# Kernel optimization log

Hardware: AMD Instinct MI355X
Metric: run time of the kernel (lower is better)

Reference implementation:

```python
import jax, jax.numpy as jnp
import numpy as np

N, E, NMASK, NC = 50000, 600000, 10000, 16
DIMS = [128, 96, 64]
EPS = 1e-5


def _sage(x, src, dst, ew, deg_pos, Wp, bp, Ws, Wn, b):
    # DGL SAGEConv 'pool': m_e = relu(fc_pool(h_src)) * w_e ; neigh = max_e->v m_e
    p = jax.nn.relu(x @ Wp.T + bp)              # [N, din]
    m = p[src] * ew[:, None]                    # [E, din]
    neigh = jax.ops.segment_max(m, dst, num_segments=N)
    neigh = jnp.where(deg_pos, neigh, 0.0)      # zero in-degree -> 0 (DGL convention)
    return jax.nn.relu(x @ Ws.T + neigh @ Wn.T + b)


def setup_inputs() -> dict:
    key = jax.random.key(0)
    ks = iter(jax.random.split(key, 64))
    inp = {}
    inp["x"] = jax.random.normal(next(ks), (N, DIMS[0]), jnp.float32)
    inp["src"] = jax.random.randint(next(ks), (E,), 0, N)
    inp["dst"] = jax.random.randint(next(ks), (E,), 0, N)
    inp["ew"] = jax.random.uniform(next(ks), (E,), jnp.float32)
    inp["mask_nodes"] = jax.random.permutation(next(ks), N)[:NMASK]
    inp["mask_token"] = jax.random.normal(next(ks), (1, DIMS[0]), jnp.float32) * 0.02

    def lin(k, o, i):
        return jax.random.normal(k, (o, i), jnp.float32) * (1.0 / np.sqrt(i))

    enc_pairs = list(zip(DIMS[:-1], DIMS[1:]))              # (128,96),(96,64)
    dec_pairs = [(o, i) for (i, o) in reversed(enc_pairs)]  # (64,96),(96,128)
    for name, pairs in (("enc", enc_pairs), ("dec", dec_pairs)):
        for l, (di, do) in enumerate(pairs):
            inp[f"{name}{l}_Wp"] = lin(next(ks), di, di)
            inp[f"{name}{l}_bp"] = jnp.zeros((di,), jnp.float32)
            inp[f"{name}{l}_Ws"] = lin(next(ks), do, di)
            inp[f"{name}{l}_Wn"] = lin(next(ks), do, di)
            inp[f"{name}{l}_b"] = jnp.zeros((do,), jnp.float32)
    H = DIMS[-1]
    inp["W_e2d"] = lin(next(ks), H, H)
    inp["Wnp"] = lin(next(ks), NC, H)
    inp["bnp"] = jnp.zeros((NC,), jnp.float32)
    inp["ln_g"] = jnp.ones((NC,), jnp.float32)
    inp["ln_b"] = jnp.zeros((NC,), jnp.float32)
    return inp


def reference(x, src, dst, ew, mask_nodes, mask_token,
              enc0_Wp, enc0_bp, enc0_Ws, enc0_Wn, enc0_b,
              enc1_Wp, enc1_bp, enc1_Ws, enc1_Wn, enc1_b,
              dec0_Wp, dec0_bp, dec0_Ws, dec0_Wn, dec0_b,
              dec1_Wp, dec1_bp, dec1_Ws, dec1_Wn, dec1_b,
              W_e2d, Wnp, bnp, ln_g, ln_b):
    deg = jax.ops.segment_sum(jnp.ones((E,), jnp.float32), dst, num_segments=N)
    deg_pos = (deg > 0)[:, None]
    # mask: out_x[mask]=0 then += enc_mask_token  ==  set to token row
    h = x.at[mask_nodes].set(mask_token[0])
    h = _sage(h, src, dst, ew, deg_pos, enc0_Wp, enc0_bp, enc0_Ws, enc0_Wn, enc0_b)
    h = _sage(h, src, dst, ew, deg_pos, enc1_Wp, enc1_bp, enc1_Ws, enc1_Wn, enc1_b)
    # dropout(p=0) is identity
    z = h @ Wnp.T + bnp                              # node_pred linear
    mu = jnp.mean(z, -1, keepdims=True)
    var = jnp.var(z, -1, keepdims=True)
    n_scores = (z - mu) * jax.lax.rsqrt(var + EPS) * ln_g + ln_b
    r = h @ W_e2d.T                                  # encoder_to_decoder (no bias)
    r = _sage(r, src, dst, ew, deg_pos, dec0_Wp, dec0_bp, dec0_Ws, dec0_Wn, dec0_b)
    r = _sage(r, src, dst, ew, deg_pos, dec1_Wp, dec1_bp, dec1_Ws, dec1_Wn, dec1_b)
    return (r[mask_nodes], x[mask_nodes], n_scores)
```

## Files before the change

kernel.cpp:

```cpp
#include <hip/hip_runtime.h>

#define EPS_LN 1e-5f

typedef __attribute__((ext_vector_type(4))) float f32x4;
typedef __attribute__((ext_vector_type(4))) int i32x4;

__device__ inline unsigned short f2bf_rne(float x) {
  unsigned int u = __float_as_uint(x);
  unsigned int r = u + 0x7fffu + ((u >> 16) & 1u);
  return (unsigned short)(r >> 16);
}

__device__ inline float4 bf4_to_f4(uint2 u) {
  float4 f;
  f.x = __uint_as_float(u.x << 16);
  f.y = __uint_as_float(u.x & 0xffff0000u);
  f.z = __uint_as_float(u.y << 16);
  f.w = __uint_as_float(u.y & 0xffff0000u);
  return f;
}

__device__ inline uint2 f4_to_bf4(float4 v) {
  uint2 o;
  o.x = (unsigned)f2bf_rne(v.x) | ((unsigned)f2bf_rne(v.y) << 16);
  o.y = (unsigned)f2bf_rne(v.z) | ((unsigned)f2bf_rne(v.w) << 16);
  return o;
}

__global__ __launch_bounds__(256) void copy_bf16_kernel(const float4* __restrict__ in,
                                                        uint2* __restrict__ out, int n4) {
  int i = blockIdx.x * 256 + threadIdx.x;
  if (i < n4) out[i] = f4_to_bf4(in[i]);
}

__global__ __launch_bounds__(256) void mask_scatter_kernel(const int* __restrict__ mn,
                                                           const float* __restrict__ token,
                                                           unsigned short* __restrict__ H,
                                                           int nmask) {
  int gid = blockIdx.x * 256 + threadIdx.x;
  if (gid >= nmask * 32) return;
  int i = gid >> 5;
  int c4 = (gid & 31) << 2;
  int r = mn[i];
  float4 t = *(const float4*)(token + c4);
  *(uint2*)(H + (size_t)r * 128 + c4) = f4_to_bf4(t);
}

__global__ __launch_bounds__(256) void hist_kernel(const int* __restrict__ dst,
                                                   int* __restrict__ deg, int nE) {
  int e = blockIdx.x * 256 + threadIdx.x;
  if (e < nE) atomicAdd(deg + dst[e], 1);
}

#define SCAN_CHUNK 1024

__global__ __launch_bounds__(256) void blocksum_kernel(const int* __restrict__ deg,
                                                       int* __restrict__ bsum, int n) {
  __shared__ int red[256];
  int base = blockIdx.x * SCAN_CHUNK;
  int tid = threadIdx.x;
  int s = 0;
#pragma unroll
  for (int t = 0; t < SCAN_CHUNK / 256; ++t) {
    int g = base + tid + t * 256;
    if (g < n) s += deg[g];
  }
  red[tid] = s;
  __syncthreads();
  for (int ofs = 128; ofs > 0; ofs >>= 1) {
    if (tid < ofs) red[tid] += red[tid + ofs];
    __syncthreads();
  }
  if (tid == 0) bsum[blockIdx.x] = red[0];
}

__global__ __launch_bounds__(64) void bscan_kernel(const int* __restrict__ bsum,
                                                   int* __restrict__ bbase,
                                                   int* __restrict__ off_n, int nb) {
  int tid = threadIdx.x;
  int v = (tid < nb) ? bsum[tid] : 0;
  int incl = v;
#pragma unroll
  for (int ofs = 1; ofs < 64; ofs <<= 1) {
    int u = __shfl_up(incl, ofs, 64);
    if (tid >= ofs) incl += u;
  }
  if (tid < nb) bbase[tid] = incl - v;
  if (tid == nb - 1) off_n[0] = incl;
}

__global__ __launch_bounds__(256) void chunkscan_kernel(const int* __restrict__ deg,
                                                        const int* __restrict__ bbase,
                                                        int* __restrict__ off, int n) {
  __shared__ int part[256];
  int tid = threadIdx.x;
  int base = blockIdx.x * SCAN_CHUNK;
  int g0 = base + tid * 4;
  int loc[4];
  int s = 0;
#pragma unroll
  for (int j = 0; j < 4; ++j) {
    int g = g0 + j;
    int d = (g < n) ? deg[g] : 0;
    loc[j] = s;
    s += d;
  }
  part[tid] = s;
  __syncthreads();
  for (int ofs = 1; ofs < 256; ofs <<= 1) {
    int v = 0;
    if (tid >= ofs) v = part[tid - ofs];
    __syncthreads();
    if (tid >= ofs) part[tid] += v;
    __syncthreads();
  }
  int pre = (tid == 0) ? 0 : part[tid - 1];
  int b = bbase[blockIdx.x] + pre;
#pragma unroll
  for (int j = 0; j < 4; ++j) {
    int g = g0 + j;
    if (g < n) off[g] = b + loc[j];
  }
}

__global__ __launch_bounds__(256) void scatter_kernel(const int* __restrict__ src,
                                                      const int* __restrict__ dst,
                                                      const float* __restrict__ ew,
                                                      const int* __restrict__ off,
                                                      int* __restrict__ cur,
                                                      int2* __restrict__ esw, int nE) {
  int e = blockIdx.x * 256 + threadIdx.x;
  if (e >= nE) return;
  int d = dst[e];
  int pos = off[d] + atomicAdd(cur + d, 1);
  esw[pos] = make_int2(src[e], __float_as_int(ew[e]));
}

__global__ __launch_bounds__(256) void neigh_csr_kernel(
    const unsigned short* __restrict__ P, const int* __restrict__ off,
    const int2* __restrict__ esw,
    unsigned short* __restrict__ neigh, int din, int lanes, int nN) {
  int gid = blockIdx.x * 256 + threadIdx.x;
  int v = gid / lanes;
  int c = (gid - v * lanes) << 3;
  if (v >= nN) return;
  int jlo = off[v], jhi = off[v + 1];
  float m[8];
#pragma unroll
  for (int t = 0; t < 8; ++t) m[t] = 0.f;
  float n1[8], n2[8], n3[8];
#pragma unroll
  for (int t = 0; t < 8; ++t) { n1[t] = 0.f; n2[t] = 0.f; n3[t] = 0.f; }
  int j = jlo;
  for (; j + 4 <= jhi; j += 4) {
    int2 e0 = esw[j], e1 = esw[j + 1], e2 = esw[j + 2], e3 = esw[j + 3];
    uint4 q0 = *(const uint4*)(P + (size_t)e0.x * din + c);
    uint4 q1 = *(const uint4*)(P + (size_t)e1.x * din + c);
    uint4 q2 = *(const uint4*)(P + (size_t)e2.x * din + c);
    uint4 q3 = *(const uint4*)(P + (size_t)e3.x * din + c);
    float w0 = __int_as_float(e0.y), w1 = __int_as_float(e1.y);
    float w2 = __int_as_float(e2.y), w3 = __int_as_float(e3.y);
    float4 a0 = bf4_to_f4(make_uint2(q0.x, q0.y)), b0 = bf4_to_f4(make_uint2(q0.z, q0.w));
    float4 a1 = bf4_to_f4(make_uint2(q1.x, q1.y)), b1 = bf4_to_f4(make_uint2(q1.z, q1.w));
    float4 a2 = bf4_to_f4(make_uint2(q2.x, q2.y)), b2 = bf4_to_f4(make_uint2(q2.z, q2.w));
    float4 a3 = bf4_to_f4(make_uint2(q3.x, q3.y)), b3 = bf4_to_f4(make_uint2(q3.z, q3.w));
    m[0] = fmaxf(m[0], a0.x * w0); m[1] = fmaxf(m[1], a0.y * w0);
    m[2] = fmaxf(m[2], a0.z * w0); m[3] = fmaxf(m[3], a0.w * w0);
    m[4] = fmaxf(m[4], b0.x * w0); m[5] = fmaxf(m[5], b0.y * w0);
    m[6] = fmaxf(m[6], b0.z * w0); m[7] = fmaxf(m[7], b0.w * w0);
    n1[0] = fmaxf(n1[0], a1.x * w1); n1[1] = fmaxf(n1[1], a1.y * w1);
    n1[2] = fmaxf(n1[2], a1.z * w1); n1[3] = fmaxf(n1[3], a1.w * w1);
    n1[4] = fmaxf(n1[4], b1.x * w1); n1[5] = fmaxf(n1[5], b1.y * w1);
    n1[6] = fmaxf(n1[6], b1.z * w1); n1[7] = fmaxf(n1[7], b1.w * w1);
    n2[0] = fmaxf(n2[0], a2.x * w2); n2[1] = fmaxf(n2[1], a2.y * w2);
    n2[2] = fmaxf(n2[2], a2.z * w2); n2[3] = fmaxf(n2[3], a2.w * w2);
    n2[4] = fmaxf(n2[4], b2.x * w2); n2[5] = fmaxf(n2[5], b2.y * w2);
    n2[6] = fmaxf(n2[6], b2.z * w2); n2[7] = fmaxf(n2[7], b2.w * w2);
    n3[0] = fmaxf(n3[0], a3.x * w3); n3[1] = fmaxf(n3[1], a3.y * w3);
    n3[2] = fmaxf(n3[2], a3.z * w3); n3[3] = fmaxf(n3[3], a3.w * w3);
    n3[4] = fmaxf(n3[4], b3.x * w3); n3[5] = fmaxf(n3[5], b3.y * w3);
    n3[6] = fmaxf(n3[6], b3.z * w3); n3[7] = fmaxf(n3[7], b3.w * w3);
  }
  for (; j < jhi; ++j) {
    int2 e = esw[j];
    float w = __int_as_float(e.y);
    uint4 q = *(const uint4*)(P + (size_t)e.x * din + c);
    float4 a = bf4_to_f4(make_uint2(q.x, q.y)), b = bf4_to_f4(make_uint2(q.z, q.w));
    m[0] = fmaxf(m[0], a.x * w); m[1] = fmaxf(m[1], a.y * w);
    m[2] = fmaxf(m[2], a.z * w); m[3] = fmaxf(m[3], a.w * w);
    m[4] = fmaxf(m[4], b.x * w); m[5] = fmaxf(m[5], b.y * w);
    m[6] = fmaxf(m[6], b.z * w); m[7] = fmaxf(m[7], b.w * w);
  }
#pragma unroll
  for (int t = 0; t < 8; ++t) m[t] = fmaxf(fmaxf(m[t], n1[t]), fmaxf(n2[t], n3[t]));
  uint2 o0 = f4_to_bf4(make_float4(m[0], m[1], m[2], m[3]));
  uint2 o1 = f4_to_bf4(make_float4(m[4], m[5], m[6], m[7]));
  *(uint4*)(neigh + (size_t)v * din + c) = make_uint4(o0.x, o0.y, o1.x, o1.y);
}

__global__ __launch_bounds__(256) void matmul_small_kernel(const float* __restrict__ A,
                                                           const float* __restrict__ B,
                                                           float* __restrict__ C,
                                                           int M, int K, int N) {
  int idx = blockIdx.x * 256 + threadIdx.x;
  if (idx >= M * N) return;
  int o = idx / N, i = idx - o * N;
  float s = 0.f;
  for (int k = 0; k < K; ++k) s += A[o * K + k] * B[k * N + i];
  C[idx] = s;
}

__device__ inline void mfma_b16(f32x4& acc, i32x4 a, i32x4 b) {
  asm volatile("v_mfma_f32_16x16x32_bf16 %0, %1, %2, %0"
               : "+v"(acc)
               : "v"(a), "v"(b));
}

__device__ inline void split_bf16(float x, unsigned short& hi, unsigned short& lo) {
  unsigned int bits = __float_as_uint(x);
  hi = (unsigned short)(bits >> 16);
  float hif = __uint_as_float((unsigned int)hi << 16);
  float res = x - hif;
  lo = (unsigned short)(__float_as_uint(res) >> 16);
}

struct SplitWArgs {
  const float* src[12];
  unsigned short* dh[12];
  unsigned short* dl[12];
  int n[12];
};

__global__ __launch_bounds__(256) void split_w_kernel(SplitWArgs a) {
  int m = blockIdx.y;
  int i = (blockIdx.x * 256 + threadIdx.x) * 4;
  if (i >= a.n[m]) return;
  float4 v = *(const float4*)(a.src[m] + i);
  unsigned short h[4], l[4];
  split_bf16(v.x, h[0], l[0]);
  split_bf16(v.y, h[1], l[1]);
  split_bf16(v.z, h[2], l[2]);
  split_bf16(v.w, h[3], l[3]);
  *(uint2*)(a.dh[m] + i) = make_uint2((unsigned)h[0] | ((unsigned)h[1] << 16),
                                      (unsigned)h[2] | ((unsigned)h[3] << 16));
  *(uint2*)(a.dl[m] + i) = make_uint2((unsigned)l[0] | ((unsigned)l[1] << 16),
                                      (unsigned)l[2] | ((unsigned)l[3] << 16));
}

template <int TNT>
__global__ __launch_bounds__(256) void mfma_gemm_kernel(
    const unsigned short* __restrict__ A1, const unsigned short* __restrict__ Wh1,
    const unsigned short* __restrict__ Wl1, int k1,
    const unsigned short* __restrict__ A2, const unsigned short* __restrict__ Wh2,
    const unsigned short* __restrict__ Wl2, int k2,
    const float* __restrict__ bias, int relu,
    unsigned short* __restrict__ C, int nrows) {
  constexpr int BN = TNT * 16;
  constexpr int WS = 136;
  __shared__ __align__(16) unsigned short Wh[BN][WS];
  __shared__ __align__(16) unsigned short Wl[BN][WS];

  const int tid = threadIdx.x;
  const int lane = tid & 63;
  const int wv = tid >> 6;
  const int lr = lane & 15;
  const int lg = lane >> 4;
  const int row0 = blockIdx.x * 64;
  const int gra = row0 + wv * 16 + lr;

  f32x4 acc[TNT];
#pragma unroll
  for (int t = 0; t < TNT; ++t) acc[t] = (f32x4)(0.f);

  for (int pass = 0; pass < 2; ++pass) {
    const unsigned short* A = pass ? A2 : A1;
    if (A == nullptr) continue;
    const unsigned short* Whp = pass ? Wh2 : Wh1;
    const unsigned short* Wlp = pass ? Wl2 : Wl1;
    const int K = pass ? k2 : k1;

    if (pass) __syncthreads();
    {
      int tot8 = BN * K / 8;
      for (int i = tid; i < tot8; i += 256) {
        int e0 = i * 8;
        int col = e0 / K;
        int kk = e0 - col * K;
        *(uint4*)&Wh[col][kk] = *(const uint4*)(Whp + e0);
        *(uint4*)&Wl[col][kk] = *(const uint4*)(Wlp + e0);
      }
    }
    __syncthreads();

    for (int cb = 0; cb < K; cb += 32) {
      i32x4 a_h = (i32x4)(0);
      if (gra < nrows) a_h = *(const i32x4*)(A + (size_t)gra * K + cb + lg * 8);
#pragma unroll
      for (int t = 0; t < TNT; ++t) {
        i32x4 b_h = *(const i32x4*)&Wh[t * 16 + lr][cb + lg * 8];
        i32x4 b_l = *(const i32x4*)&Wl[t * 16 + lr][cb + lg * 8];
        mfma_b16(acc[t], a_h, b_h);
        mfma_b16(acc[t], a_h, b_l);
      }
    }
  }

  asm volatile("s_nop 7\n\ts_nop 7" ::);

#pragma unroll
  for (int t = 0; t < TNT; ++t) {
    int c = t * 16 + lr;
    float bv = bias ? bias[c] : 0.f;
#pragma unroll
    for (int q = 0; q < 4; ++q) {
      int r = row0 + wv * 16 + lg * 4 + q;
      if (r < nrows) {
        float v = acc[t][q] + bv;
        if (relu) v = fmaxf(v, 0.f);
        C[(size_t)r * BN + c] = f2bf_rne(v);
      }
    }
  }
}

__global__ __launch_bounds__(256) void nodepred_ln_kernel(
    const unsigned short* __restrict__ H, const float* __restrict__ Wnp,
    const float* __restrict__ bnp, const float* __restrict__ g,
    const float* __restrict__ lb, float* __restrict__ out, int nrows) {
  __shared__ float hs[16][64];
  int tid = threadIdx.x;
  int row0 = blockIdx.x * 16;
  {
    int r = tid >> 4;
    int c4 = (tid & 15) << 2;
    int gr = row0 + r;
    float4 v = make_float4(0.f, 0.f, 0.f, 0.f);
    if (gr < nrows) v = bf4_to_f4(*(const uint2*)(H + (size_t)gr * 64 + c4));
    *(float4*)&hs[r][c4] = v;
  }
  __syncthreads();
  int r = tid >> 4, j = tid & 15;
  float z = bnp[j];
  const float* wrow = Wnp + j * 64;
#pragma unroll 8
  for (int k = 0; k < 64; ++k) z += hs[r][k] * wrow[k];
  float s = z, s2 = z * z;
#pragma unroll
  for (int m = 1; m < 16; m <<= 1) {
    s += __shfl_xor(s, m, 16);
    s2 += __shfl_xor(s2, m, 16);
  }
  float mu = s * (1.f / 16.f);
  float var = s2 * (1.f / 16.f) - mu * mu;
  float o = (z - mu) * rsqrtf(var + EPS_LN) * g[j] + lb[j];
  int gr = row0 + r;
  if (gr < nrows) out[(size_t)gr * 16 + j] = o;
}

__global__ __launch_bounds__(256) void gather_out_kernel(
    const int* __restrict__ mn, const unsigned short* __restrict__ R,
    const float* __restrict__ X,
    float* __restrict__ o1, float* __restrict__ o2, int nmask) {
  int gid = blockIdx.x * 256 + threadIdx.x;
  if (gid >= nmask * 32) return;
  int i = gid >> 5, c4 = (gid & 31) << 2;
  int r = mn[i];
  float4 rv = bf4_to_f4(*(const uint2*)(R + (size_t)r * 128 + c4));
  *(float4*)(o1 + (size_t)i * 128 + c4) = rv;
  *(float4*)(o2 + (size_t)i * 128 + c4) = *(const float4*)(X + (size_t)r * 128 + c4);
}

static void launch_gemm(const unsigned short* A1, const unsigned short* Wh1,
                        const unsigned short* Wl1, int k1,
                        const unsigned short* A2, const unsigned short* Wh2,
                        const unsigned short* Wl2, int k2,
                        const float* bias, int relu,
                        unsigned short* C, int m, int nrows, hipStream_t s) {
  int blocks = (nrows + 63) / 64;
  switch (m) {
    case 128:
      mfma_gemm_kernel<8><<<blocks, 256, 0, s>>>(A1, Wh1, Wl1, k1, A2, Wh2, Wl2, k2,
                                                 bias, relu, C, nrows);
      break;
    case 96:
      mfma_gemm_kernel<6><<<blocks, 256, 0, s>>>(A1, Wh1, Wl1, k1, A2, Wh2, Wl2, k2,
                                                 bias, relu, C, nrows);
      break;
    case 64:
      mfma_gemm_kernel<4><<<blocks, 256, 0, s>>>(A1, Wh1, Wl1, k1, A2, Wh2, Wl2, k2,
                                                 bias, relu, C, nrows);
      break;
  }
}

extern "C" void kernel_launch(void* const* d_in, const int* in_sizes, int n_in,
                              void* d_out, int out_size, void* d_ws, size_t ws_size,
                              hipStream_t stream) {
  const float* x = (const float*)d_in[0];
  const int* src = (const int*)d_in[1];
  const int* dst = (const int*)d_in[2];
  const float* ew = (const float*)d_in[3];
  const int* mn = (const int*)d_in[4];
  const float* token = (const float*)d_in[5];

  const float* W[20];
  for (int i = 0; i < 20; ++i) W[i] = (const float*)d_in[6 + i];
  const float* W_e2d = (const float*)d_in[26];
  const float* Wnp = (const float*)d_in[27];
  const float* bnp = (const float*)d_in[28];
  const float* ln_g = (const float*)d_in[29];
  const float* ln_b = (const float*)d_in[30];

  const int Nn = in_sizes[0] / 128;
  const int E = in_sizes[1];
  const int nmask = in_sizes[4];
  const int nb = (Nn + SCAN_CHUNK - 1) / SCAN_CHUNK;

  unsigned short* bufA = (unsigned short*)d_ws;
  unsigned short* bufB = bufA + (size_t)Nn * 128;
  unsigned short* pool16 = bufB + (size_t)Nn * 128;
  unsigned short* neigh16 = pool16 + (size_t)Nn * 128;
  int* deg = (int*)(neigh16 + (size_t)Nn * 128);
  int* cur = deg + Nn;
  int2* esw = (int2*)(cur + Nn);
  int* off = (int*)(esw + E);
  int* bsum = off + Nn + 1;
  int* bbase = bsum + 64;
  float* WpP = (float*)(bbase + 64);
  float* WsP = WpP + 64 * 64;
  unsigned short* wplanes =
      (unsigned short*)(((uintptr_t)(WsP + 96 * 64) + 15) & ~(uintptr_t)15);

  matmul_small_kernel<<<(64 * 64 + 255) / 256, 256, 0, stream>>>(W[10], W_e2d, WpP, 64, 64, 64);
  matmul_small_kernel<<<(96 * 64 + 255) / 256, 256, 0, stream>>>(W[12], W_e2d, WsP, 96, 64, 64);

  const int msz[12] = {128 * 128, 96 * 128, 96 * 128, 96 * 96, 64 * 96, 64 * 96,
                       64 * 64,  96 * 64,  96 * 64,  96 * 96, 128 * 96, 128 * 96};
  const float* msrc[12] = {W[0], W[2], W[3], W[5], W[7], W[8],
                           WpP,  WsP,  W[13], W[15], W[17], W[18]};
  int mtot = 0;
  int moff[12];
  for (int i = 0; i < 12; ++i) { moff[i] = mtot; mtot += msz[i]; }
  unsigned short* wh_[12];
  unsigned short* wl_[12];
  SplitWArgs sa;
  for (int i = 0; i < 12; ++i) {
    wh_[i] = wplanes + moff[i];
    wl_[i] = wplanes + mtot + moff[i];
    sa.src[i] = msrc[i];
    sa.dh[i] = wh_[i];
    sa.dl[i] = wl_[i];
    sa.n[i] = msz[i];
  }
  {
    dim3 grid((128 * 128 / 4 + 255) / 256, 12);
    split_w_kernel<<<grid, 256, 0, stream>>>(sa);
  }

  hipMemsetAsync(deg, 0, (size_t)Nn * 2 * sizeof(int), stream);
  hist_kernel<<<(E + 255) / 256, 256, 0, stream>>>(dst, deg, E);
  blocksum_kernel<<<nb, 256, 0, stream>>>(deg, bsum, Nn);
  bscan_kernel<<<1, 64, 0, stream>>>(bsum, bbase, off + Nn, nb);
  chunkscan_kernel<<<nb, 256, 0, stream>>>(deg, bbase, off, Nn);
  scatter_kernel<<<(E + 255) / 256, 256, 0, stream>>>(src, dst, ew, off, cur, esw, E);

  {
    int n4 = Nn * 128 / 4;
    copy_bf16_kernel<<<(n4 + 255) / 256, 256, 0, stream>>>((const float4*)x, (uint2*)bufA, n4);
    mask_scatter_kernel<<<(nmask * 32 + 255) / 256, 256, 0, stream>>>(mn, token, bufA, nmask);
  }

  auto run_sage = [&](int ip, int is, int in_, const float* bp, const float* b,
                      int din, int dout) {
    launch_gemm(bufA, wh_[ip], wl_[ip], din, nullptr, nullptr, nullptr, 0,
                bp, 1, pool16, din, Nn, stream);
    int lanes = din >> 3;
    long long tot = (long long)Nn * lanes;
    int nblocks = (int)((tot + 255) / 256);
    neigh_csr_kernel<<<nblocks, 256, 0, stream>>>(pool16, off, esw, neigh16, din, lanes, Nn);
    launch_gemm(bufA, wh_[is], wl_[is], din, neigh16, wh_[in_], wl_[in_], din,
                b, 1, bufB, dout, Nn, stream);
    unsigned short* t = bufA; bufA = bufB; bufB = t;
  };

  run_sage(0, 1, 2, W[1], W[4], 128, 96);
  run_sage(3, 4, 5, W[6], W[9], 96, 64);

  float* out_r = (float*)d_out;
  float* out_x = out_r + (size_t)nmask * 128;
  float* out_ns = out_x + (size_t)nmask * 128;
  nodepred_ln_kernel<<<(Nn + 15) / 16, 256, 0, stream>>>(bufA, Wnp, bnp, ln_g, ln_b, out_ns, Nn);

  run_sage(6, 7, 8, W[11], W[14], 64, 96);
  run_sage(9, 10, 11, W[16], W[19], 96, 128);

  gather_out_kernel<<<(nmask * 32 + 255) / 256, 256, 0, stream>>>(mn, bufA, x, out_r, out_x, nmask);
}
```

Baseline: 369.1 us.

## Fuse next layer's pool GEMM into combine GEMM and merge prep kernels

Each SAGE layer's combine GEMM now also computes the next layer's pooling projection (relu(h Wp^T + bp)) from the rows it just wrote, so a separate pool GEMM launch is gone and the output tile is re-read while likely still in cache. Several small preprocessing kernels (bf16 copy, histogram, small weight products, block sums, mask scatter, weight splitting) are merged into two multi-role launches to cut launch overhead. The fused epilogue re-reads C from global memory after a threadfence and reloads shared weights, which adds a sync and extra work per block; the chained-kernel fusion also drops flexibility (bias/relu always applied).

```diff
diff --git a/kernel.cpp b/kernel.cpp
--- a/kernel.cpp
+++ b/kernel.cpp
@@ -27,51 +27,129 @@
   return o;
 }
 
-__global__ __launch_bounds__(256) void copy_bf16_kernel(const float4* __restrict__ in,
-                                                        uint2* __restrict__ out, int n4) {
-  int i = blockIdx.x * 256 + threadIdx.x;
-  if (i < n4) out[i] = f4_to_bf4(in[i]);
-}
-
-__global__ __launch_bounds__(256) void mask_scatter_kernel(const int* __restrict__ mn,
-                                                           const float* __restrict__ token,
-                                                           unsigned short* __restrict__ H,
-                                                           int nmask) {
-  int gid = blockIdx.x * 256 + threadIdx.x;
-  if (gid >= nmask * 32) return;
-  int i = gid >> 5;
-  int c4 = (gid & 31) << 2;
-  int r = mn[i];
-  float4 t = *(const float4*)(token + c4);
-  *(uint2*)(H + (size_t)r * 128 + c4) = f4_to_bf4(t);
-}
-
-__global__ __launch_bounds__(256) void hist_kernel(const int* __restrict__ dst,
-                                                   int* __restrict__ deg, int nE) {
-  int e = blockIdx.x * 256 + threadIdx.x;
-  if (e < nE) atomicAdd(deg + dst[e], 1);
+__device__ inline void split_bf16(float x, unsigned short& hi, unsigned short& lo) {
+  unsigned int bits = __float_as_uint(x);
+  hi = (unsigned short)(bits >> 16);
+  float hif = __uint_as_float((unsigned int)hi << 16);
+  float res = x - hif;
+  lo = (unsigned short)(__float_as_uint(res) >> 16);
+}
+
+__device__ inline void mfma_b16(f32x4& acc, i32x4 a, i32x4 b) {
+  asm volatile("v_mfma_f32_16x16x32_bf16 %0, %1, %2, %0"
+               : "+v"(acc)
+               : "v"(a), "v"(b));
+}
+
+struct SplitWArgs {
+  const float* src[12];
+  unsigned short* dh[12];
+  unsigned short* dl[12];
+  int n[12];
+};
+
+struct Prep1Args {
+  const float4* x4; uint2* h_out; int n4; int cb_blocks;
+  const int* dst; int* deg; int nE; int hist_blocks;
+  const float* W10; const float* We2d; float* WpP;
+  const float* W12; float* WsP;
+};
+
+__global__ __launch_bounds__(256) void prep1_kernel(Prep1Args a) {
+  int b = blockIdx.x;
+  int tid = threadIdx.x;
+  if (b < a.cb_blocks) {
+    int i = b * 256 + tid;
+    if (i < a.n4) a.h_out[i] = f4_to_bf4(a.x4[i]);
+    return;
+  }
+  b -= a.cb_blocks;
+  if (b < a.hist_blocks) {
+    int e = b * 256 + tid;
+    if (e < a.nE) atomicAdd(a.deg + a.dst[e], 1);
+    return;
+  }
+  b -= a.hist_blocks;
+  if (b < 16) {
+    int idx = b * 256 + tid;
+    if (idx < 64 * 64) {
+      int o = idx >> 6, i = idx & 63;
+      float s = 0.f;
+      for (int k = 0; k < 64; ++k) s += a.W10[o * 64 + k] * a.We2d[k * 64 + i];
+      a.WpP[idx] = s;
+    }
+    return;
+  }
+  b -= 16;
+  {
+    int idx = b * 256 + tid;
+    if (idx < 96 * 64) {
+      int o = idx >> 6, i = idx & 63;
+      float s = 0.f;
+      for (int k = 0; k < 64; ++k) s += a.W12[o * 64 + k] * a.We2d[k * 64 + i];
+      a.WsP[idx] = s;
+    }
+  }
 }
 
 #define SCAN_CHUNK 1024
 
-__global__ __launch_bounds__(256) void blocksum_kernel(const int* __restrict__ deg,
-                                                       int* __restrict__ bsum, int n) {
+struct Prep2Args {
+  const int* deg; int* bsum; int n; int nb;
+  const int* mn; const float* token; unsigned short* H; int nmask; int ms_blocks;
+  SplitWArgs sw;
+  int boff[13];
+};
+
+__global__ __launch_bounds__(256) void prep2_kernel(Prep2Args a) {
   __shared__ int red[256];
-  int base = blockIdx.x * SCAN_CHUNK;
+  int b = blockIdx.x;
   int tid = threadIdx.x;
-  int s = 0;
-#pragma unroll
-  for (int t = 0; t < SCAN_CHUNK / 256; ++t) {
-    int g = base + tid + t * 256;
-    if (g < n) s += deg[g];
-  }
-  red[tid] = s;
-  __syncthreads();
-  for (int ofs = 128; ofs > 0; ofs >>= 1) {
-    if (tid < ofs) red[tid] += red[tid + ofs];
+  if (b < a.nb) {
+    int base = b * SCAN_CHUNK;
+    int s = 0;
+#pragma unroll
+    for (int t = 0; t < SCAN_CHUNK / 256; ++t) {
+      int g = base + tid + t * 256;
+      if (g < a.n) s += a.deg[g];
+    }
+    red[tid] = s;
     __syncthreads();
-  }
-  if (tid == 0) bsum[blockIdx.x] = red[0];
+    for (int ofs = 128; ofs > 0; ofs >>= 1) {
+      if (tid < ofs) red[tid] += red[tid + ofs];
+      __syncthreads();
+    }
+    if (tid == 0) a.bsum[b] = red[0];
+    return;
+  }
+  b -= a.nb;
+  if (b < a.ms_blocks) {
+    int gid = b * 256 + tid;
+    if (gid >= a.nmask * 32) return;
+    int i = gid >> 5;
+    int c4 = (gid & 31) << 2;
+    int r = a.mn[i];
+    float4 t = *(const float4*)(a.token + c4);
+    *(uint2*)(a.H + (size_t)r * 128 + c4) = f4_to_bf4(t);
+    return;
+  }
+  b -= a.ms_blocks;
+  {
+    int m = 0;
+    while (m < 11 && b >= a.boff[m + 1]) ++m;
+    int i = ((b - a.boff[m]) * 256 + tid) * 4;
+    if (i >= a.sw.n[m]) return;
+    float4 v = *(const float4*)(a.sw.src[m] + i);
+    unsigned short h[4], l[4];
+    split_bf16(v.x, h[0], l[0]);
+    split_bf16(v.y, h[1], l[1]);
+    split_bf16(v.z, h[2], l[2]);
+    split_bf16(v.w, h[3], l[3]);
+    *(uint2*)(a.sw.dh[m] + i) = make_uint2((unsigned)h[0] | ((unsigned)h[1] << 16),
+                                           (unsigned)h[2] | ((unsigned)h[3] << 16));
+    *(uint2*)(a.sw.dl[m] + i) = make_uint2((unsigned)l[0] | ((unsigned)l[1] << 16),
+                                           (unsigned)l[2] | ((unsigned)l[3] << 16));
+  }
 }
 
 __global__ __launch_bounds__(64) void bscan_kernel(const int* __restrict__ bsum,
@@ -198,62 +276,11 @@
   *(uint4*)(neigh + (size_t)v * din + c) = make_uint4(o0.x, o0.y, o1.x, o1.y);
 }
 
-__global__ __launch_bounds__(256) void matmul_small_kernel(const float* __restrict__ A,
-                                                           const float* __restrict__ B,
-                                                           float* __restrict__ C,
-                                                           int M, int K, int N) {
-  int idx = blockIdx.x * 256 + threadIdx.x;
-  if (idx >= M * N) return;
-  int o = idx / N, i = idx - o * N;
-  float s = 0.f;
-  for (int k = 0; k < K; ++k) s += A[o * K + k] * B[k * N + i];
-  C[idx] = s;
-}
-
-__device__ inline void mfma_b16(f32x4& acc, i32x4 a, i32x4 b) {
-  asm volatile("v_mfma_f32_16x16x32_bf16 %0, %1, %2, %0"
-               : "+v"(acc)
-               : "v"(a), "v"(b));
-}
-
-__device__ inline void split_bf16(float x, unsigned short& hi, unsigned short& lo) {
-  unsigned int bits = __float_as_uint(x);
-  hi = (unsigned short)(bits >> 16);
-  float hif = __uint_as_float((unsigned int)hi << 16);
-  float res = x - hif;
-  lo = (unsigned short)(__float_as_uint(res) >> 16);
-}
-
-struct SplitWArgs {
-  const float* src[12];
-  unsigned short* dh[12];
-  unsigned short* dl[12];
-  int n[12];
-};
-
-__global__ __launch_bounds__(256) void split_w_kernel(SplitWArgs a) {
-  int m = blockIdx.y;
-  int i = (blockIdx.x * 256 + threadIdx.x) * 4;
-  if (i >= a.n[m]) return;
-  float4 v = *(const float4*)(a.src[m] + i);
-  unsigned short h[4], l[4];
-  split_bf16(v.x, h[0], l[0]);
-  split_bf16(v.y, h[1], l[1]);
-  split_bf16(v.z, h[2], l[2]);
-  split_bf16(v.w, h[3], l[3]);
-  *(uint2*)(a.dh[m] + i) = make_uint2((unsigned)h[0] | ((unsigned)h[1] << 16),
-                                      (unsigned)h[2] | ((unsigned)h[3] << 16));
-  *(uint2*)(a.dl[m] + i) = make_uint2((unsigned)l[0] | ((unsigned)l[1] << 16),
-                                      (unsigned)l[2] | ((unsigned)l[3] << 16));
-}
-
 template <int TNT>
 __global__ __launch_bounds__(256) void mfma_gemm_kernel(
     const unsigned short* __restrict__ A1, const unsigned short* __restrict__ Wh1,
     const unsigned short* __restrict__ Wl1, int k1,
-    const unsigned short* __restrict__ A2, const unsigned short* __restrict__ Wh2,
-    const unsigned short* __restrict__ Wl2, int k2,
-    const float* __restrict__ bias, int relu,
+    const float* __restrict__ bias,
     unsigned short* __restrict__ C, int nrows) {
   constexpr int BN = TNT * 16;
   constexpr int WS = 136;
@@ -272,12 +299,78 @@
 #pragma unroll
   for (int t = 0; t < TNT; ++t) acc[t] = (f32x4)(0.f);
 
+  {
+    int tot8 = BN * k1 / 8;
+    for (int i = tid; i < tot8; i += 256) {
+      int e0 = i * 8;
+      int col = e0 / k1;
+      int kk = e0 - col * k1;
+      *(uint4*)&Wh[col][kk] = *(const uint4*)(Wh1 + e0);
+      *(uint4*)&Wl[col][kk] = *(const uint4*)(Wl1 + e0);
+    }
+  }
+  __syncthreads();
+
+  for (int cb = 0; cb < k1; cb += 32) {
+    i32x4 a_h = (i32x4)(0);
+    if (gra < nrows) a_h = *(const i32x4*)(A1 + (size_t)gra * k1 + cb + lg * 8);
+#pragma unroll
+    for (int t = 0; t < TNT; ++t) {
+      i32x4 b_h = *(const i32x4*)&Wh[t * 16 + lr][cb + lg * 8];
+      i32x4 b_l = *(const i32x4*)&Wl[t * 16 + lr][cb + lg * 8];
+      mfma_b16(acc[t], a_h, b_h);
+      mfma_b16(acc[t], a_h, b_l);
+    }
+  }
+
+  asm volatile("s_nop 7\n\ts_nop 7" ::);
+
+#pragma unroll
+  for (int t = 0; t < TNT; ++t) {
+    int c = t * 16 + lr;
+    float bv = bias[c];
+#pragma unroll
+    for (int q = 0; q < 4; ++q) {
+      int r = row0 + wv * 16 + lg * 4 + q;
+      if (r < nrows) {
+        float v = fmaxf(acc[t][q] + bv, 0.f);
+        C[(size_t)r * BN + c] = f2bf_rne(v);
+      }
+    }
+  }
+}
+
+template <int TNT>
+__global__ __launch_bounds__(256) void mfma_gemm_fused_kernel(
+    const unsigned short* __restrict__ A1, const unsigned short* __restrict__ Wh1,
+    const unsigned short* __restrict__ Wl1,
+    const unsigned short* __restrict__ A2, const unsigned short* __restrict__ Wh2,
+    const unsigned short* __restrict__ Wl2, int K,
+    const float* __restrict__ bias, unsigned short* __restrict__ C,
+    const unsigned short* __restrict__ pWh, const unsigned short* __restrict__ pWl,
+    const float* __restrict__ pBias, unsigned short* __restrict__ P_out,
+    int nrows) {
+  constexpr int BN = TNT * 16;
+  constexpr int WS = 136;
+  __shared__ __align__(16) unsigned short Wh[BN][WS];
+  __shared__ __align__(16) unsigned short Wl[BN][WS];
+
+  const int tid = threadIdx.x;
+  const int lane = tid & 63;
+  const int wv = tid >> 6;
+  const int lr = lane & 15;
+  const int lg = lane >> 4;
+  const int row0 = blockIdx.x * 64;
+  const int gra = row0 + wv * 16 + lr;
+
+  f32x4 acc[TNT];
+#pragma unroll
+  for (int t = 0; t < TNT; ++t) acc[t] = (f32x4)(0.f);
+
   for (int pass = 0; pass < 2; ++pass) {
     const unsigned short* A = pass ? A2 : A1;
-    if (A == nullptr) continue;
     const unsigned short* Whp = pass ? Wh2 : Wh1;
     const unsigned short* Wlp = pass ? Wl2 : Wl1;
-    const int K = pass ? k2 : k1;
 
     if (pass) __syncthreads();
     {
@@ -310,14 +403,60 @@
 #pragma unroll
   for (int t = 0; t < TNT; ++t) {
     int c = t * 16 + lr;
-    float bv = bias ? bias[c] : 0.f;
+    float bv = bias[c];
 #pragma unroll
     for (int q = 0; q < 4; ++q) {
       int r = row0 + wv * 16 + lg * 4 + q;
       if (r < nrows) {
-        float v = acc[t][q] + bv;
-        if (relu) v = fmaxf(v, 0.f);
+        float v = fmaxf(acc[t][q] + bv, 0.f);
         C[(size_t)r * BN + c] = f2bf_rne(v);
+      }
+    }
+  }
+
+  if (P_out == nullptr) return;
+
+  __threadfence();
+  __syncthreads();
+  {
+    int tot8 = BN * BN / 8;
+    for (int i = tid; i < tot8; i += 256) {
+      int e0 = i * 8;
+      int col = e0 / BN;
+      int kk = e0 - col * BN;
+      *(uint4*)&Wh[col][kk] = *(const uint4*)(pWh + e0);
+      *(uint4*)&Wl[col][kk] = *(const uint4*)(pWl + e0);
+    }
+  }
+  __syncthreads();
+
+#pragma unroll
+  for (int t = 0; t < TNT; ++t) acc[t] = (f32x4)(0.f);
+
+  for (int cb = 0; cb < BN; cb += 32) {
+    i32x4 a_h = (i32x4)(0);
+    if (gra < nrows) a_h = *(const i32x4*)(C + (size_t)gra * BN + cb + lg * 8);
+#pragma unroll
+    for (int t = 0; t < TNT; ++t) {
+      i32x4 b_h = *(const i32x4*)&Wh[t * 16 + lr][cb + lg * 8];
+      i32x4 b_l = *(const i32x4*)&Wl[t * 16 + lr][cb + lg * 8];
+      mfma_b16(acc[t], a_h, b_h);
+      mfma_b16(acc[t], a_h, b_l);
+    }
+  }
+
+  asm volatile("s_nop 7\n\ts_nop 7" ::);
+
+#pragma unroll
+  for (int t = 0; t < TNT; ++t) {
+    int c = t * 16 + lr;
+    float bv = pBias[c];
+#pragma unroll
+    for (int q = 0; q < 4; ++q) {
+      int r = row0 + wv * 16 + lg * 4 + q;
+      if (r < nrows) {
+        float v = fmaxf(acc[t][q] + bv, 0.f);
+        P_out[(size_t)r * BN + c] = f2bf_rne(v);
       }
     }
   }
@@ -370,25 +509,27 @@
   *(float4*)(o2 + (size_t)i * 128 + c4) = *(const float4*)(X + (size_t)r * 128 + c4);
 }
 
-static void launch_gemm(const unsigned short* A1, const unsigned short* Wh1,
-                        const unsigned short* Wl1, int k1,
-                        const unsigned short* A2, const unsigned short* Wh2,
-                        const unsigned short* Wl2, int k2,
-                        const float* bias, int relu,
-                        unsigned short* C, int m, int nrows, hipStream_t s) {
+static void launch_fused(const unsigned short* A1, const unsigned short* Wh1,
+                         const unsigned short* Wl1,
+                         const unsigned short* A2, const unsigned short* Wh2,
+                         const unsigned short* Wl2, int K,
+                         const float* bias, unsigned short* C,
+                         const unsigned short* pWh, const unsigned short* pWl,
+                         const float* pBias, unsigned short* P_out,
+                         int m, int nrows, hipStream_t s) {
   int blocks = (nrows + 63) / 64;
   switch (m) {
     case 128:
-      mfma_gemm_kernel<8><<<blocks, 256, 0, s>>>(A1, Wh1, Wl1, k1, A2, Wh2, Wl2, k2,
-                                                 bias, relu, C, nrows);
+      mfma_gemm_fused_kernel<8><<<blocks, 256, 0, s>>>(A1, Wh1, Wl1, A2, Wh2, Wl2, K,
+                                                       bias, C, pWh, pWl, pBias, P_out, nrows);
       break;
     case 96:
-      mfma_gemm_kernel<6><<<blocks, 256, 0, s>>>(A1, Wh1, Wl1, k1, A2, Wh2, Wl2, k2,
-                                                 bias, relu, C, nrows);
+      mfma_gemm_fused_kernel<6><<<blocks, 256, 0, s>>>(A1, Wh1, Wl1, A2, Wh2, Wl2, K,
+                                                       bias, C, pWh, pWl, pBias, P_out, nrows);
       break;
     case 64:
-      mfma_gemm_kernel<4><<<blocks, 256, 0, s>>>(A1, Wh1, Wl1, k1, A2, Wh2, Wl2, k2,
-                                                 bias, relu, C, nrows);
+      mfma_gemm_fused_kernel<4><<<blocks, 256, 0, s>>>(A1, Wh1, Wl1, A2, Wh2, Wl2, K,
+                                                       bias, C, pWh, pWl, pBias, P_out, nrows);
       break;
   }
 }
@@ -431,9 +572,6 @@
   unsigned short* wplanes =
       (unsigned short*)(((uintptr_t)(WsP + 96 * 64) + 15) & ~(uintptr_t)15);
 
-  matmul_small_kernel<<<(64 * 64 + 255) / 256, 256, 0, stream>>>(W[10], W_e2d, WpP, 64, 64, 64);
-  matmul_small_kernel<<<(96 * 64 + 255) / 256, 256, 0, stream>>>(W[12], W_e2d, WsP, 96, 64, 64);
-
   const int msz[12] = {128 * 128, 96 * 128, 96 * 128, 96 * 96, 64 * 96, 64 * 96,
                        64 * 64,  96 * 64,  96 * 64,  96 * 96, 128 * 96, 128 * 96};
   const float* msrc[12] = {W[0], W[2], W[3], W[5], W[7], W[8],
@@ -443,56 +581,78 @@
   for (int i = 0; i < 12; ++i) { moff[i] = mtot; mtot += msz[i]; }
   unsigned short* wh_[12];
   unsigned short* wl_[12];
-  SplitWArgs sa;
   for (int i = 0; i < 12; ++i) {
     wh_[i] = wplanes + moff[i];
     wl_[i] = wplanes + mtot + moff[i];
-    sa.src[i] = msrc[i];
-    sa.dh[i] = wh_[i];
-    sa.dl[i] = wl_[i];
-    sa.n[i] = msz[i];
-  }
-  {
-    dim3 grid((128 * 128 / 4 + 255) / 256, 12);
-    split_w_kernel<<<grid, 256, 0, stream>>>(sa);
   }
 
   hipMemsetAsync(deg, 0, (size_t)Nn * 2 * sizeof(int), stream);
-  hist_kernel<<<(E + 255) / 256, 256, 0, stream>>>(dst, deg, E);
-  blocksum_kernel<<<nb, 256, 0, stream>>>(deg, bsum, Nn);
+
+  Prep1Args p1;
+  p1.x4 = (const float4*)x;
+  p1.h_out = (uint2*)bufA;
+  p1.n4 = Nn * 128 / 4;
+  p1.cb_blocks = (p1.n4 + 255) / 256;
+  p1.dst = dst;
+  p1.deg = deg;
+  p1.nE = E;
+  p1.hist_blocks = (E + 255) / 256;
+  p1.W10 = W[10]; p1.We2d = W_e2d; p1.WpP = WpP;
+  p1.W12 = W[12]; p1.WsP = WsP;
+  int p1_blocks = p1.cb_blocks + p1.hist_blocks + 16 + 24;
+  prep1_kernel<<<p1_blocks, 256, 0, stream>>>(p1);
+
+  Prep2Args p2;
+  p2.deg = deg; p2.bsum = bsum; p2.n = Nn; p2.nb = nb;
+  p2.mn = mn; p2.token = token; p2.H = bufA; p2.nmask = nmask;
+  p2.ms_blocks = (nmask * 32 + 255) / 256;
+  for (int i = 0; i < 12; ++i) {
+    p2.sw.src[i] = msrc[i];
+    p2.sw.dh[i] = wh_[i];
+    p2.sw.dl[i] = wl_[i];
+    p2.sw.n[i] = msz[i];
+  }
+  p2.boff[0] = 0;
+  for (int i = 0; i < 12; ++i) p2.boff[i + 1] = p2.boff[i] + (msz[i] / 4 + 255) / 256;
+  int p2_blocks = p2.nb + p2.ms_blocks + p2.boff[12];
+  prep2_kernel<<<p2_blocks, 256, 0, stream>>>(p2);
+
   bscan_kernel<<<1, 64, 0, stream>>>(bsum, bbase, off + Nn, nb);
   chunkscan_kernel<<<nb, 256, 0, stream>>>(deg, bbase, off, Nn);
   scatter_kernel<<<(E + 255) / 256, 256, 0, stream>>>(src, dst, ew, off, cur, esw, E);
 
-  {
-    int n4 = Nn * 128 / 4;
-    copy_bf16_kernel<<<(n4 + 255) / 256, 256, 0, stream>>>((const float4*)x, (uint2*)bufA, n4);
-    mask_scatter_kernel<<<(nmask * 32 + 255) / 256, 256, 0, stream>>>(mn, token, bufA, nmask);
-  }
-
-  auto run_sage = [&](int ip, int is, int in_, const float* bp, const float* b,
-                      int din, int dout) {
-    launch_gemm(bufA, wh_[ip], wl_[ip], din, nullptr, nullptr, nullptr, 0,
-                bp, 1, pool16, din, Nn, stream);
+  int gblocks = (Nn + 63) / 64;
+
+  mfma_gemm_kernel<8><<<gblocks, 256, 0, stream>>>(bufA, wh_[0], wl_[0], 128, W[1],
+                                                   pool16, Nn);
+
+  auto neigh = [&](int din) {
     int lanes = din >> 3;
     long long tot = (long long)Nn * lanes;
     int nblocks = (int)((tot + 255) / 256);
     neigh_csr_kernel<<<nblocks, 256, 0, stream>>>(pool16, off, esw, neigh16, din, lanes, Nn);
-    launch_gemm(bufA, wh_[is], wl_[is], din, neigh16, wh_[in_], wl_[in_], din,
-                b, 1, bufB, dout, Nn, stream);
-    unsigned short* t = bufA; bufA = bufB; bufB = t;
   };
 
-  run_sage(0, 1, 2, W[1], W[4], 128, 96);
-  run_sage(3, 4, 5, W[6], W[9], 96, 64);
+  neigh(128);
+  launch_fused(bufA, wh_[1], wl_[1], neigh16, wh_[2], wl_[2], 128, W[4], bufB,
+               wh_[3], wl_[3], W[6], pool16, 96, Nn, stream);
+
+  neigh(96);
+  launch_fused(bufB, wh_[4], wl_[4], neigh16, wh_[5], wl_[5], 96, W[9], bufA,
+               wh_[6], wl_[6], W[11], pool16, 64, Nn, stream);
 
   float* out_r = (float*)d_out;
   float* out_x = out_r + (size_t)nmask * 128;
   float* out_ns = out_x + (size_t)nmask * 128;
   nodepred_ln_kernel<<<(Nn + 15) / 16, 256, 0, stream>>>(bufA, Wnp, bnp, ln_g, ln_b, out_ns, Nn);
 
-  run_sage(6, 7, 8, W[11], W[14], 64, 96);
-  run_sage(9, 10, 11, W[16], W[19], 96, 128);
+  neigh(64);
+  launch_fused(bufA, wh_[7], wl_[7], neigh16, wh_[8], wl_[8], 64, W[14], bufB,
+               wh_[9], wl_[9], W[16], pool16, 96, Nn, stream);
+
+  neigh(96);
+  launch_fused(bufB, wh_[10], wl_[10], neigh16, wh_[11], wl_[11], 96, W[19], bufA,
+               nullptr, nullptr, nullptr, nullptr, 128, Nn, stream);
 
   gather_out_kernel<<<(nmask * 32 + 255) / 256, 256, 0, stream>>>(mn, bufA, x, out_r, out_x, nmask);
 }
```

Measured after the change: 536.9 us. 1.45x slower.
